# Performance work log

Hardware: AMD Instinct MI355X
Metric: run time of the kernel (lower is better)

Reference implementation:

```python
import jax, jax.numpy as jnp
import numpy as np

D = 128
SCALE = 1.0 / np.sqrt(D)  # scalar_value


def setup_inputs() -> dict:
    key = jax.random.key(0)
    k1, k2, k3 = jax.random.split(key, 3)
    B, N, S = 2, 16, 2048
    q = jax.random.normal(k1, (B, N, S, D), dtype=jnp.float32)
    k = jax.random.normal(k2, (B, N, S, D), dtype=jnp.float32)
    v = jax.random.normal(k3, (B, N, S, D), dtype=jnp.float32)
    return {"q": q, "k": k, "v": v}


def reference(q, k, v):
    # BNSD layout. scores = scale * Q K^T, causal mask, softmax with
    # explicit max/sum tracking (golden for NPU fusion attention).
    s1, s2 = q.shape[2], k.shape[2]
    scores = jnp.einsum('bnsd,bntd->bnst', q, k) * SCALE
    # generate_attn_mask: causal (lower-triangular kept), masked -> -inf
    causal = jnp.triu(jnp.ones((s1, s2), dtype=bool), k=1)
    scores = jnp.where(causal, -jnp.inf, scores)
    softmax_max = jnp.max(scores, axis=-1, keepdims=True)          # [B,N,S,1]
    exp_scores = jnp.exp(scores - softmax_max)
    softmax_sum = jnp.sum(exp_scores, axis=-1, keepdims=True)      # [B,N,S,1]
    softmax_res = exp_scores / softmax_sum
    out = jnp.einsum('bnst,bntd->bnsd', softmax_res, v)
    # NPU golden repeats stats x8 along last dim
    return (out,
            jnp.tile(softmax_max, (1, 1, 1, 8)),
            jnp.tile(softmax_sum, (1, 1, 1, 8)))
```

## Files before the change

### kernel.cpp

```cpp
#include <hip/hip_runtime.h>
#include <math.h>
#include <stdint.h>

#define D_DIM 128
#define SEQ 2048
#define NHEADS 32
#define BC 64
#define SCALE 0.08838834764831843f

typedef short bf16x8 __attribute__((ext_vector_type(8)));
typedef float f32x4 __attribute__((ext_vector_type(4)));

union Frag { uint32_t u[4]; bf16x8 v; unsigned short s[8]; };
union Pack8 { unsigned short s[8]; uint4 q; };

__device__ __forceinline__ uint32_t fbits(float x) { return __builtin_bit_cast(uint32_t, x); }
__device__ __forceinline__ float bbits(uint32_t u) { return __builtin_bit_cast(float, u); }
__device__ __forceinline__ unsigned short bf16_rne(float x) {
    uint32_t u = fbits(x);
    u += 0x7FFFu + ((u >> 16) & 1u);
    return (unsigned short)(u >> 16);
}
__device__ __forceinline__ void split2(float a, float b, uint32_t& hp, uint32_t& lp) {
    uint32_t ua = fbits(a) & 0xFFFF0000u, ub = fbits(b) & 0xFFFF0000u;
    float la = a - bbits(ua), lb = b - bbits(ub);
    hp = (ua >> 16) | ub;
    lp = (fbits(la) >> 16) | (fbits(lb) & 0xFFFF0000u);
}

__global__ __launch_bounds__(512, 2) void fa_fused(
    const float* __restrict__ q, const float* __restrict__ k,
    const float* __restrict__ v, float* __restrict__ out)
{
    __shared__ __align__(16) unsigned short Khs[64 * 128];
    __shared__ __align__(16) unsigned short Kls[64 * 128];
    __shared__ __align__(16) unsigned short Vhs[128 * 64];
    __shared__ __align__(16) unsigned short Pbs[128 * 64];

    const int x  = blockIdx.x;
    const int xi = x >> 5;
    const int it = (x < 256) ? (15 - xi) : (xi - 8);
    const int h  = x & 31;

    const int t    = (int)threadIdx.x;
    const int wb   = t >> 6;
    const int lane = t & 63;
    const int ln   = lane & 15;
    const int qd   = lane >> 4;

    const float* qh = q + (size_t)h * SEQ * D_DIM;
    const float* kh = k + (size_t)h * SEQ * D_DIM;
    const float* vh = v + (size_t)h * SEQ * D_DIM;
    float* out_o = out;
    float* out_m = out + (size_t)NHEADS * SEQ * D_DIM;
    float* out_l = out_m + (size_t)NHEADS * SEQ * 8;

    const int qrow0 = it * 128 + wb * 16;

    const int krow0 = t >> 5;
    const int kd4   = t & 31;
    const int vcc   = wb;
    const int vd0   = lane;

    Frag Qh[4], Ql[4];
    {
        const float* qp = qh + (size_t)(qrow0 + ln) * D_DIM;
        #pragma unroll
        for (int kc = 0; kc < 4; ++kc) {
            const int kb = kc * 32 + qd * 8;
            float e[8];
            *(float4*)(e)     = *(const float4*)(qp + kb);
            *(float4*)(e + 4) = *(const float4*)(qp + kb + 4);
            #pragma unroll
            for (int j = 0; j < 8; ++j) e[j] *= SCALE;
            #pragma unroll
            for (int j = 0; j < 4; ++j)
                split2(e[2 * j], e[2 * j + 1], Qh[kc].u[j], Ql[kc].u[j]);
        }
    }

    float4 kreg[4];
    float  vraw[2][8];
    uint2  khi[4], klo[4];
    uint4  vcv[2];

    #pragma unroll
    for (int itr = 0; itr < 4; ++itr)
        kreg[itr] = *(const float4*)(kh + (size_t)(itr * 16 + krow0) * D_DIM + kd4 * 4);
    #pragma unroll
    for (int uu = 0; uu < 2; ++uu) {
        const int d = uu * 64 + vd0;
        #pragma unroll
        for (int j = 0; j < 8; ++j)
            vraw[uu][j] = vh[(size_t)(vcc * 8 + j) * D_DIM + d];
    }
    #pragma unroll
    for (int itr = 0; itr < 4; ++itr) {
        uint32_t hp0, lp0, hp1, lp1;
        split2(kreg[itr].x, kreg[itr].y, hp0, lp0);
        split2(kreg[itr].z, kreg[itr].w, hp1, lp1);
        khi[itr] = make_uint2(hp0, hp1);
        klo[itr] = make_uint2(lp0, lp1);
    }
    #pragma unroll
    for (int uu = 0; uu < 2; ++uu) {
        Pack8 p8;
        #pragma unroll
        for (int j = 0; j < 8; ++j) p8.s[j] = bf16_rne(vraw[uu][j]);
        vcv[uu] = p8.q;
    }

    f32x4 accO[8];
    float m_r[4], l_r[4];
    #pragma unroll
    for (int nd = 0; nd < 8; ++nd) accO[nd] = (f32x4){0.f, 0.f, 0.f, 0.f};
    #pragma unroll
    for (int r = 0; r < 4; ++r) { m_r[r] = -INFINITY; l_r[r] = 0.f; }

    const int jt_end = 2 * it + 1;
    for (int jt = 0; jt <= jt_end; ++jt) {
        const int c0 = jt * BC;

        __syncthreads();

        #pragma unroll
        for (int itr = 0; itr < 4; ++itr) {
            const int row = itr * 16 + krow0;
            const int off = row * 128 + (((kd4 >> 1) ^ (row & 7)) * 8) + (kd4 & 1) * 4;
            *(uint2*)(Khs + off) = khi[itr];
            *(uint2*)(Kls + off) = klo[itr];
        }
        #pragma unroll
        for (int uu = 0; uu < 2; ++uu) {
            const int d = uu * 64 + vd0;
            *(uint4*)(Vhs + d * 64 + ((vcc ^ (d & 7)) * 8)) = vcv[uu];
        }

        __syncthreads();

        if (jt < jt_end) {
            const int c0n = c0 + BC;
            const float* kp2 = kh + (size_t)c0n * D_DIM;
            #pragma unroll
            for (int itr = 0; itr < 4; ++itr)
                kreg[itr] = *(const float4*)(kp2 + (size_t)(itr * 16 + krow0) * D_DIM + kd4 * 4);
            #pragma unroll
            for (int uu = 0; uu < 2; ++uu) {
                const int d = uu * 64 + vd0;
                #pragma unroll
                for (int j = 0; j < 8; ++j)
                    vraw[uu][j] = vh[(size_t)(c0n + vcc * 8 + j) * D_DIM + d];
            }
        }

        if (c0 <= qrow0 + 15) {
            f32x4 accS[4];
            #pragma unroll
            for (int nt = 0; nt < 4; ++nt) accS[nt] = (f32x4){0.f, 0.f, 0.f, 0.f};
            #pragma unroll
            for (int kc = 0; kc < 4; ++kc) {
                #pragma unroll
                for (int nt = 0; nt < 4; ++nt) {
                    int n = nt * 16 + ln;
                    int off = n * 128 + (((kc * 4 + qd) ^ (n & 7)) * 8);
                    Frag Bh, Bl;
                    Bh.v = *(const bf16x8*)(Khs + off);
                    Bl.v = *(const bf16x8*)(Kls + off);
                    f32x4 c = accS[nt];
                    c = __builtin_amdgcn_mfma_f32_16x16x32_bf16(Qh[kc].v, Bh.v, c, 0, 0, 0);
                    c = __builtin_amdgcn_mfma_f32_16x16x32_bf16(Qh[kc].v, Bl.v, c, 0, 0, 0);
                    c = __builtin_amdgcn_mfma_f32_16x16x32_bf16(Ql[kc].v, Bh.v, c, 0, 0, 0);
                    accS[nt] = c;
                }
            }
            const bool needMask = (c0 + 63 > qrow0);
            float mxr[4];
            #pragma unroll
            for (int r = 0; r < 4; ++r) {
                const int rowg = qrow0 + qd * 4 + r;
                float mx = -INFINITY;
                #pragma unroll
                for (int nt = 0; nt < 4; ++nt) {
                    float s = accS[nt][r];
                    if (needMask && (c0 + nt * 16 + ln > rowg)) s = -INFINITY;
                    accS[nt][r] = s;
                    mx = fmaxf(mx, s);
                }
                mxr[r] = mx;
            }
            #pragma unroll
            for (int r = 0; r < 4; ++r) {
                #pragma unroll
                for (int off = 1; off < 16; off <<= 1) mxr[r] = fmaxf(mxr[r], __shfl_xor(mxr[r], off));
            }
            const bool grow = (mxr[0] > m_r[0]) | (mxr[1] > m_r[1]) |
                              (mxr[2] > m_r[2]) | (mxr[3] > m_r[3]);
            if (__any(grow)) {
                #pragma unroll
                for (int r = 0; r < 4; ++r) {
                    const float mnew = fmaxf(m_r[r], mxr[r]);
                    const float alpha = __expf(m_r[r] - mnew);
                    m_r[r] = mnew;
                    l_r[r] *= alpha;
                    #pragma unroll
                    for (int nd = 0; nd < 8; ++nd) accO[nd][r] *= alpha;
                }
            }
            #pragma unroll
            for (int r = 0; r < 4; ++r) {
                float p[4];
                #pragma unroll
                for (int nt = 0; nt < 4; ++nt) p[nt] = __expf(accS[nt][r] - m_r[r]);
                l_r[r] += (p[0] + p[1]) + (p[2] + p[3]);
                const int R = wb * 16 + qd * 4 + r;
                #pragma unroll
                for (int nt = 0; nt < 4; ++nt) {
                    int c = nt * 16 + ln;
                    Pbs[R * 64 + (((c >> 3) ^ (R & 7)) * 8) + (c & 7)] = bf16_rne(p[nt]);
                }
            }
            #pragma unroll
            for (int kc2 = 0; kc2 < 2; ++kc2) {
                Frag Pf;
                const int R = wb * 16 + ln;
                Pf.v = *(const bf16x8*)(Pbs + R * 64 + (((kc2 * 4 + qd) ^ (R & 7)) * 8));
                #pragma unroll
                for (int nd = 0; nd < 8; ++nd) {
                    int dcol = nd * 16 + ln;
                    int voff = dcol * 64 + (((kc2 * 4 + qd) ^ (dcol & 7)) * 8);
                    Frag Vh2;
                    Vh2.v = *(const bf16x8*)(Vhs + voff);
                    accO[nd] = __builtin_amdgcn_mfma_f32_16x16x32_bf16(Pf.v, Vh2.v, accO[nd], 0, 0, 0);
                }
            }
        }

        if (jt < jt_end) {
            #pragma unroll
            for (int itr = 0; itr < 4; ++itr) {
                uint32_t hp0, lp0, hp1, lp1;
                split2(kreg[itr].x, kreg[itr].y, hp0, lp0);
                split2(kreg[itr].z, kreg[itr].w, hp1, lp1);
                khi[itr] = make_uint2(hp0, hp1);
                klo[itr] = make_uint2(lp0, lp1);
            }
            #pragma unroll
            for (int uu = 0; uu < 2; ++uu) {
                Pack8 p8;
                #pragma unroll
                for (int j = 0; j < 8; ++j) p8.s[j] = bf16_rne(vraw[uu][j]);
                vcv[uu] = p8.q;
            }
        }
    }

    #pragma unroll
    for (int r = 0; r < 4; ++r) {
        #pragma unroll
        for (int off = 1; off < 16; off <<= 1) l_r[r] += __shfl_xor(l_r[r], off);
    }
    #pragma unroll
    for (int r = 0; r < 4; ++r) {
        const int rowg = qrow0 + qd * 4 + r;
        const float invl = 1.0f / l_r[r];
        float* op = out_o + (size_t)h * SEQ * D_DIM + (size_t)rowg * D_DIM;
        #pragma unroll
        for (int nd = 0; nd < 8; ++nd) op[nd * 16 + ln] = accO[nd][r] * invl;
        if (ln < 8) {
            size_t sb = ((size_t)h * SEQ + rowg) * 8 + ln;
            out_m[sb] = m_r[r];
            out_l[sb] = l_r[r];
        }
    }
}

extern "C" void kernel_launch(void* const* d_in, const int* in_sizes, int n_in,
                              void* d_out, int out_size, void* d_ws, size_t ws_size,
                              hipStream_t stream) {
    const float* q = (const float*)d_in[0];
    const float* k = (const float*)d_in[1];
    const float* v = (const float*)d_in[2];
    float* out = (float*)d_out;
    (void)d_ws; (void)ws_size;

    fa_fused<<<dim3(512), dim3(512), 0, stream>>>(q, k, v, out);
}
```

Before: 275.9 us.

## Double-buffer K/V tiles in LDS and pair causal query tiles per block

Each block now handles two query tiles (it = 15-xi and xi) in sequence, so every block does equal causal work, and the grid shrinks from 512 to 256 blocks. K/V shared-memory tiles are double-buffered so the next tile is written into the alternate buffer during compute, cutting the per-iteration barriers from two to one. LDS use grows by about 48KB per block, which may lower occupancy from the requested two blocks per CU. The smaller grid may also leave some CUs less loaded.

```diff
diff --git a/kernel.cpp b/kernel.cpp
--- a/kernel.cpp
+++ b/kernel.cpp
@@ -32,14 +32,13 @@
     const float* __restrict__ q, const float* __restrict__ k,
     const float* __restrict__ v, float* __restrict__ out)
 {
-    __shared__ __align__(16) unsigned short Khs[64 * 128];
-    __shared__ __align__(16) unsigned short Kls[64 * 128];
-    __shared__ __align__(16) unsigned short Vhs[128 * 64];
+    __shared__ __align__(16) unsigned short KhsB[2][64 * 128];
+    __shared__ __align__(16) unsigned short KlsB[2][64 * 128];
+    __shared__ __align__(16) unsigned short VhsB[2][128 * 64];
     __shared__ __align__(16) unsigned short Pbs[128 * 64];
 
     const int x  = blockIdx.x;
     const int xi = x >> 5;
-    const int it = (x < 256) ? (15 - xi) : (xi - 8);
     const int h  = x & 31;
 
     const int t    = (int)threadIdx.x;
@@ -55,221 +54,246 @@
     float* out_m = out + (size_t)NHEADS * SEQ * D_DIM;
     float* out_l = out_m + (size_t)NHEADS * SEQ * 8;
 
-    const int qrow0 = it * 128 + wb * 16;
-
     const int krow0 = t >> 5;
     const int kd4   = t & 31;
     const int vcc   = wb;
     const int vd0   = lane;
 
-    Frag Qh[4], Ql[4];
-    {
-        const float* qp = qh + (size_t)(qrow0 + ln) * D_DIM;
-        #pragma unroll
-        for (int kc = 0; kc < 4; ++kc) {
-            const int kb = kc * 32 + qd * 8;
-            float e[8];
-            *(float4*)(e)     = *(const float4*)(qp + kb);
-            *(float4*)(e + 4) = *(const float4*)(qp + kb + 4);
-            #pragma unroll
-            for (int j = 0; j < 8; ++j) e[j] *= SCALE;
-            #pragma unroll
-            for (int j = 0; j < 4; ++j)
-                split2(e[2 * j], e[2 * j + 1], Qh[kc].u[j], Ql[kc].u[j]);
-        }
-    }
-
-    float4 kreg[4];
-    float  vraw[2][8];
-    uint2  khi[4], klo[4];
-    uint4  vcv[2];
-
-    #pragma unroll
-    for (int itr = 0; itr < 4; ++itr)
-        kreg[itr] = *(const float4*)(kh + (size_t)(itr * 16 + krow0) * D_DIM + kd4 * 4);
-    #pragma unroll
-    for (int uu = 0; uu < 2; ++uu) {
-        const int d = uu * 64 + vd0;
-        #pragma unroll
-        for (int j = 0; j < 8; ++j)
-            vraw[uu][j] = vh[(size_t)(vcc * 8 + j) * D_DIM + d];
-    }
-    #pragma unroll
-    for (int itr = 0; itr < 4; ++itr) {
-        uint32_t hp0, lp0, hp1, lp1;
-        split2(kreg[itr].x, kreg[itr].y, hp0, lp0);
-        split2(kreg[itr].z, kreg[itr].w, hp1, lp1);
-        khi[itr] = make_uint2(hp0, hp1);
-        klo[itr] = make_uint2(lp0, lp1);
-    }
-    #pragma unroll
-    for (int uu = 0; uu < 2; ++uu) {
-        Pack8 p8;
-        #pragma unroll
-        for (int j = 0; j < 8; ++j) p8.s[j] = bf16_rne(vraw[uu][j]);
-        vcv[uu] = p8.q;
-    }
-
-    f32x4 accO[8];
-    float m_r[4], l_r[4];
-    #pragma unroll
-    for (int nd = 0; nd < 8; ++nd) accO[nd] = (f32x4){0.f, 0.f, 0.f, 0.f};
-    #pragma unroll
-    for (int r = 0; r < 4; ++r) { m_r[r] = -INFINITY; l_r[r] = 0.f; }
-
-    const int jt_end = 2 * it + 1;
-    for (int jt = 0; jt <= jt_end; ++jt) {
-        const int c0 = jt * BC;
-
-        __syncthreads();
-
-        #pragma unroll
-        for (int itr = 0; itr < 4; ++itr) {
-            const int row = itr * 16 + krow0;
-            const int off = row * 128 + (((kd4 >> 1) ^ (row & 7)) * 8) + (kd4 & 1) * 4;
-            *(uint2*)(Khs + off) = khi[itr];
-            *(uint2*)(Kls + off) = klo[itr];
-        }
+    for (int ph = 0; ph < 2; ++ph) {
+        const int it = ph ? xi : (15 - xi);
+        const int qrow0 = it * 128 + wb * 16;
+
+        Frag Qh[4], Ql[4];
+        {
+            const float* qp = qh + (size_t)(qrow0 + ln) * D_DIM;
+            #pragma unroll
+            for (int kc = 0; kc < 4; ++kc) {
+                const int kb = kc * 32 + qd * 8;
+                float e[8];
+                *(float4*)(e)     = *(const float4*)(qp + kb);
+                *(float4*)(e + 4) = *(const float4*)(qp + kb + 4);
+                #pragma unroll
+                for (int j = 0; j < 8; ++j) e[j] *= SCALE;
+                #pragma unroll
+                for (int j = 0; j < 4; ++j)
+                    split2(e[2 * j], e[2 * j + 1], Qh[kc].u[j], Ql[kc].u[j]);
+            }
+        }
+
+        float4 kreg[4];
+        float  vraw[2][8];
+        uint2  khi[4], klo[4];
+        uint4  vcv[2];
+
+        #pragma unroll
+        for (int itr = 0; itr < 4; ++itr)
+            kreg[itr] = *(const float4*)(kh + (size_t)(itr * 16 + krow0) * D_DIM + kd4 * 4);
         #pragma unroll
         for (int uu = 0; uu < 2; ++uu) {
             const int d = uu * 64 + vd0;
-            *(uint4*)(Vhs + d * 64 + ((vcc ^ (d & 7)) * 8)) = vcv[uu];
-        }
-
-        __syncthreads();
-
-        if (jt < jt_end) {
-            const int c0n = c0 + BC;
-            const float* kp2 = kh + (size_t)c0n * D_DIM;
-            #pragma unroll
-            for (int itr = 0; itr < 4; ++itr)
-                kreg[itr] = *(const float4*)(kp2 + (size_t)(itr * 16 + krow0) * D_DIM + kd4 * 4);
+            #pragma unroll
+            for (int j = 0; j < 8; ++j)
+                vraw[uu][j] = vh[(size_t)(vcc * 8 + j) * D_DIM + d];
+        }
+        #pragma unroll
+        for (int itr = 0; itr < 4; ++itr) {
+            uint32_t hp0, lp0, hp1, lp1;
+            split2(kreg[itr].x, kreg[itr].y, hp0, lp0);
+            split2(kreg[itr].z, kreg[itr].w, hp1, lp1);
+            khi[itr] = make_uint2(hp0, hp1);
+            klo[itr] = make_uint2(lp0, lp1);
+        }
+        #pragma unroll
+        for (int uu = 0; uu < 2; ++uu) {
+            Pack8 p8;
+            #pragma unroll
+            for (int j = 0; j < 8; ++j) p8.s[j] = bf16_rne(vraw[uu][j]);
+            vcv[uu] = p8.q;
+        }
+        {
+            unsigned short* Kh0 = KhsB[0];
+            unsigned short* Kl0 = KlsB[0];
+            unsigned short* Vh0 = VhsB[0];
+            #pragma unroll
+            for (int itr = 0; itr < 4; ++itr) {
+                const int row = itr * 16 + krow0;
+                const int off = row * 128 + (((kd4 >> 1) ^ (row & 7)) * 8) + (kd4 & 1) * 4;
+                *(uint2*)(Kh0 + off) = khi[itr];
+                *(uint2*)(Kl0 + off) = klo[itr];
+            }
             #pragma unroll
             for (int uu = 0; uu < 2; ++uu) {
                 const int d = uu * 64 + vd0;
-                #pragma unroll
-                for (int j = 0; j < 8; ++j)
-                    vraw[uu][j] = vh[(size_t)(c0n + vcc * 8 + j) * D_DIM + d];
-            }
-        }
-
-        if (c0 <= qrow0 + 15) {
-            f32x4 accS[4];
-            #pragma unroll
-            for (int nt = 0; nt < 4; ++nt) accS[nt] = (f32x4){0.f, 0.f, 0.f, 0.f};
-            #pragma unroll
-            for (int kc = 0; kc < 4; ++kc) {
-                #pragma unroll
-                for (int nt = 0; nt < 4; ++nt) {
-                    int n = nt * 16 + ln;
-                    int off = n * 128 + (((kc * 4 + qd) ^ (n & 7)) * 8);
-                    Frag Bh, Bl;
-                    Bh.v = *(const bf16x8*)(Khs + off);
-                    Bl.v = *(const bf16x8*)(Kls + off);
-                    f32x4 c = accS[nt];
-                    c = __builtin_amdgcn_mfma_f32_16x16x32_bf16(Qh[kc].v, Bh.v, c, 0, 0, 0);
-                    c = __builtin_amdgcn_mfma_f32_16x16x32_bf16(Qh[kc].v, Bl.v, c, 0, 0, 0);
-                    c = __builtin_amdgcn_mfma_f32_16x16x32_bf16(Ql[kc].v, Bh.v, c, 0, 0, 0);
-                    accS[nt] = c;
-                }
-            }
-            const bool needMask = (c0 + 63 > qrow0);
-            float mxr[4];
-            #pragma unroll
-            for (int r = 0; r < 4; ++r) {
-                const int rowg = qrow0 + qd * 4 + r;
-                float mx = -INFINITY;
-                #pragma unroll
-                for (int nt = 0; nt < 4; ++nt) {
-                    float s = accS[nt][r];
-                    if (needMask && (c0 + nt * 16 + ln > rowg)) s = -INFINITY;
-                    accS[nt][r] = s;
-                    mx = fmaxf(mx, s);
-                }
-                mxr[r] = mx;
-            }
-            #pragma unroll
-            for (int r = 0; r < 4; ++r) {
-                #pragma unroll
-                for (int off = 1; off < 16; off <<= 1) mxr[r] = fmaxf(mxr[r], __shfl_xor(mxr[r], off));
-            }
-            const bool grow = (mxr[0] > m_r[0]) | (mxr[1] > m_r[1]) |
-                              (mxr[2] > m_r[2]) | (mxr[3] > m_r[3]);
-            if (__any(grow)) {
+                *(uint4*)(Vh0 + d * 64 + ((vcc ^ (d & 7)) * 8)) = vcv[uu];
+            }
+        }
+        __syncthreads();
+
+        f32x4 accO[8];
+        float m_r[4], l_r[4];
+        #pragma unroll
+        for (int nd = 0; nd < 8; ++nd) accO[nd] = (f32x4){0.f, 0.f, 0.f, 0.f};
+        #pragma unroll
+        for (int r = 0; r < 4; ++r) { m_r[r] = -INFINITY; l_r[r] = 0.f; }
+
+        const int jt_end = 2 * it + 1;
+        for (int jt = 0; jt <= jt_end; ++jt) {
+            const int c0  = jt * BC;
+            const int cur = jt & 1;
+
+            if (jt < jt_end) {
+                const int c0n = c0 + BC;
+                const float* kp2 = kh + (size_t)c0n * D_DIM;
+                #pragma unroll
+                for (int itr = 0; itr < 4; ++itr)
+                    kreg[itr] = *(const float4*)(kp2 + (size_t)(itr * 16 + krow0) * D_DIM + kd4 * 4);
+                #pragma unroll
+                for (int uu = 0; uu < 2; ++uu) {
+                    const int d = uu * 64 + vd0;
+                    #pragma unroll
+                    for (int j = 0; j < 8; ++j)
+                        vraw[uu][j] = vh[(size_t)(c0n + vcc * 8 + j) * D_DIM + d];
+                }
+            }
+
+            if (c0 <= qrow0 + 15) {
+                const unsigned short* Khs = KhsB[cur];
+                const unsigned short* Kls = KlsB[cur];
+                const unsigned short* Vhs = VhsB[cur];
+                f32x4 accS[4];
+                #pragma unroll
+                for (int nt = 0; nt < 4; ++nt) accS[nt] = (f32x4){0.f, 0.f, 0.f, 0.f};
+                #pragma unroll
+                for (int kc = 0; kc < 4; ++kc) {
+                    #pragma unroll
+                    for (int nt = 0; nt < 4; ++nt) {
+                        int n = nt * 16 + ln;
+                        int off = n * 128 + (((kc * 4 + qd) ^ (n & 7)) * 8);
+                        Frag Bh, Bl;
+                        Bh.v = *(const bf16x8*)(Khs + off);
+                        Bl.v = *(const bf16x8*)(Kls + off);
+                        f32x4 c = accS[nt];
+                        c = __builtin_amdgcn_mfma_f32_16x16x32_bf16(Qh[kc].v, Bh.v, c, 0, 0, 0);
+                        c = __builtin_amdgcn_mfma_f32_16x16x32_bf16(Qh[kc].v, Bl.v, c, 0, 0, 0);
+                        c = __builtin_amdgcn_mfma_f32_16x16x32_bf16(Ql[kc].v, Bh.v, c, 0, 0, 0);
+                        accS[nt] = c;
+                    }
+                }
+                const bool needMask = (c0 + 63 > qrow0);
+                float mxr[4];
                 #pragma unroll
                 for (int r = 0; r < 4; ++r) {
-                    const float mnew = fmaxf(m_r[r], mxr[r]);
-                    const float alpha = __expf(m_r[r] - mnew);
-                    m_r[r] = mnew;
-                    l_r[r] *= alpha;
-                    #pragma unroll
-                    for (int nd = 0; nd < 8; ++nd) accO[nd][r] *= alpha;
-                }
-            }
-            #pragma unroll
-            for (int r = 0; r < 4; ++r) {
-                float p[4];
-                #pragma unroll
-                for (int nt = 0; nt < 4; ++nt) p[nt] = __expf(accS[nt][r] - m_r[r]);
-                l_r[r] += (p[0] + p[1]) + (p[2] + p[3]);
-                const int R = wb * 16 + qd * 4 + r;
-                #pragma unroll
-                for (int nt = 0; nt < 4; ++nt) {
-                    int c = nt * 16 + ln;
-                    Pbs[R * 64 + (((c >> 3) ^ (R & 7)) * 8) + (c & 7)] = bf16_rne(p[nt]);
-                }
-            }
-            #pragma unroll
-            for (int kc2 = 0; kc2 < 2; ++kc2) {
-                Frag Pf;
-                const int R = wb * 16 + ln;
-                Pf.v = *(const bf16x8*)(Pbs + R * 64 + (((kc2 * 4 + qd) ^ (R & 7)) * 8));
-                #pragma unroll
-                for (int nd = 0; nd < 8; ++nd) {
-                    int dcol = nd * 16 + ln;
-                    int voff = dcol * 64 + (((kc2 * 4 + qd) ^ (dcol & 7)) * 8);
-                    Frag Vh2;
-                    Vh2.v = *(const bf16x8*)(Vhs + voff);
-                    accO[nd] = __builtin_amdgcn_mfma_f32_16x16x32_bf16(Pf.v, Vh2.v, accO[nd], 0, 0, 0);
-                }
-            }
-        }
-
-        if (jt < jt_end) {
-            #pragma unroll
-            for (int itr = 0; itr < 4; ++itr) {
-                uint32_t hp0, lp0, hp1, lp1;
-                split2(kreg[itr].x, kreg[itr].y, hp0, lp0);
-                split2(kreg[itr].z, kreg[itr].w, hp1, lp1);
-                khi[itr] = make_uint2(hp0, hp1);
-                klo[itr] = make_uint2(lp0, lp1);
-            }
-            #pragma unroll
-            for (int uu = 0; uu < 2; ++uu) {
-                Pack8 p8;
-                #pragma unroll
-                for (int j = 0; j < 8; ++j) p8.s[j] = bf16_rne(vraw[uu][j]);
-                vcv[uu] = p8.q;
-            }
-        }
-    }
-
-    #pragma unroll
-    for (int r = 0; r < 4; ++r) {
-        #pragma unroll
-        for (int off = 1; off < 16; off <<= 1) l_r[r] += __shfl_xor(l_r[r], off);
-    }
-    #pragma unroll
-    for (int r = 0; r < 4; ++r) {
-        const int rowg = qrow0 + qd * 4 + r;
-        const float invl = 1.0f / l_r[r];
-        float* op = out_o + (size_t)h * SEQ * D_DIM + (size_t)rowg * D_DIM;
-        #pragma unroll
-        for (int nd = 0; nd < 8; ++nd) op[nd * 16 + ln] = accO[nd][r] * invl;
-        if (ln < 8) {
-            size_t sb = ((size_t)h * SEQ + rowg) * 8 + ln;
-            out_m[sb] = m_r[r];
-            out_l[sb] = l_r[r];
+                    const int rowg = qrow0 + qd * 4 + r;
+                    float mx = -INFINITY;
+                    #pragma unroll
+                    for (int nt = 0; nt < 4; ++nt) {
+                        float s = accS[nt][r];
+                        if (needMask && (c0 + nt * 16 + ln > rowg)) s = -INFINITY;
+                        accS[nt][r] = s;
+                        mx = fmaxf(mx, s);
+                    }
+                    mxr[r] = mx;
+                }
+                #pragma unroll
+                for (int r = 0; r < 4; ++r) {
+                    #pragma unroll
+                    for (int off = 1; off < 16; off <<= 1) mxr[r] = fmaxf(mxr[r], __shfl_xor(mxr[r], off));
+                }
+                const bool grow = (mxr[0] > m_r[0]) | (mxr[1] > m_r[1]) |
+                                  (mxr[2] > m_r[2]) | (mxr[3] > m_r[3]);
+                if (__any(grow)) {
+                    #pragma unroll
+                    for (int r = 0; r < 4; ++r) {
+                        const float mnew = fmaxf(m_r[r], mxr[r]);
+                        const float alpha = __expf(m_r[r] - mnew);
+                        m_r[r] = mnew;
+                        l_r[r] *= alpha;
+                        #pragma unroll
+                        for (int nd = 0; nd < 8; ++nd) accO[nd][r] *= alpha;
+                    }
+                }
+                #pragma unroll
+                for (int r = 0; r < 4; ++r) {
+                    float p[4];
+                    #pragma unroll
+                    for (int nt = 0; nt < 4; ++nt) p[nt] = __expf(accS[nt][r] - m_r[r]);
+                    l_r[r] += (p[0] + p[1]) + (p[2] + p[3]);
+                    const int R = wb * 16 + qd * 4 + r;
+                    #pragma unroll
+                    for (int nt = 0; nt < 4; ++nt) {
+                        int c = nt * 16 + ln;
+                        Pbs[R * 64 + (((c >> 3) ^ (R & 7)) * 8) + (c & 7)] = bf16_rne(p[nt]);
+                    }
+                }
+                #pragma unroll
+                for (int kc2 = 0; kc2 < 2; ++kc2) {
+                    Frag Pf;
+                    const int R = wb * 16 + ln;
+                    Pf.v = *(const bf16x8*)(Pbs + R * 64 + (((kc2 * 4 + qd) ^ (R & 7)) * 8));
+                    #pragma unroll
+                    for (int nd = 0; nd < 8; ++nd) {
+                        int dcol = nd * 16 + ln;
+                        int voff = dcol * 64 + (((kc2 * 4 + qd) ^ (dcol & 7)) * 8);
+                        Frag Vh2;
+                        Vh2.v = *(const bf16x8*)(Vhs + voff);
+                        accO[nd] = __builtin_amdgcn_mfma_f32_16x16x32_bf16(Pf.v, Vh2.v, accO[nd], 0, 0, 0);
+                    }
+                }
+            }
+
+            if (jt < jt_end) {
+                #pragma unroll
+                for (int itr = 0; itr < 4; ++itr) {
+                    uint32_t hp0, lp0, hp1, lp1;
+                    split2(kreg[itr].x, kreg[itr].y, hp0, lp0);
+                    split2(kreg[itr].z, kreg[itr].w, hp1, lp1);
+                    khi[itr] = make_uint2(hp0, hp1);
+                    klo[itr] = make_uint2(lp0, lp1);
+                }
+                #pragma unroll
+                for (int uu = 0; uu < 2; ++uu) {
+                    Pack8 p8;
+                    #pragma unroll
+                    for (int j = 0; j < 8; ++j) p8.s[j] = bf16_rne(vraw[uu][j]);
+                    vcv[uu] = p8.q;
+                }
+                unsigned short* Khn = KhsB[cur ^ 1];
+                unsigned short* Kln = KlsB[cur ^ 1];
+                unsigned short* Vhn = VhsB[cur ^ 1];
+                #pragma unroll
+                for (int itr = 0; itr < 4; ++itr) {
+                    const int row = itr * 16 + krow0;
+                    const int off = row * 128 + (((kd4 >> 1) ^ (row & 7)) * 8) + (kd4 & 1) * 4;
+                    *(uint2*)(Khn + off) = khi[itr];
+                    *(uint2*)(Kln + off) = klo[itr];
+                }
+                #pragma unroll
+                for (int uu = 0; uu < 2; ++uu) {
+                    const int d = uu * 64 + vd0;
+                    *(uint4*)(Vhn + d * 64 + ((vcc ^ (d & 7)) * 8)) = vcv[uu];
+                }
+            }
+
+            __syncthreads();
+        }
+
+        #pragma unroll
+        for (int r = 0; r < 4; ++r) {
+            #pragma unroll
+            for (int off = 1; off < 16; off <<= 1) l_r[r] += __shfl_xor(l_r[r], off);
+        }
+        #pragma unroll
+        for (int r = 0; r < 4; ++r) {
+            const int rowg = qrow0 + qd * 4 + r;
+            const float invl = 1.0f / l_r[r];
+            float* op = out_o + (size_t)h * SEQ * D_DIM + (size_t)rowg * D_DIM;
+            #pragma unroll
+            for (int nd = 0; nd < 8; ++nd) op[nd * 16 + ln] = accO[nd][r] * invl;
+            if (ln < 8) {
+                size_t sb = ((size_t)h * SEQ + rowg) * 8 + ln;
+                out_m[sb] = m_r[r];
+                out_l[sb] = l_r[r];
+            }
         }
     }
 }
@@ -283,5 +307,5 @@
     float* out = (float*)d_out;
     (void)d_ws; (void)ws_size;
 
-    fa_fused<<<dim3(512), dim3(512), 0, stream>>>(q, k, v, out);
+    fa_fused<<<dim3(256), dim3(512), 0, stream>>>(q, k, v, out);
 }
```

After: 227.1 us. -17.7%, faster.
